# Kernel optimization log

Measured on AMD Instinct MI355X. Metric: run time of the kernel, lower is better.

Reference implementation:

```python
import jax, jax.numpy as jnp
import numpy as np

RADIUS = 4
SIGMA_I = 10.0
SIGMA_X = 4.0
NUM_CLASSES = 8
PAD = RADIUS - 1          # 3, ConstantPad3d(radius-1, eps)
WIN = 2 * PAD + 1         # 7x7x7 window
EPS = float(np.finfo(np.float64).eps)


def _dist_flat():
    # spatial gaussian, zero outside the ball x^2+y^2+z^2 < radius^2
    r = np.arange(1 - RADIUS, RADIUS)
    xx, yy, zz = np.meshgrid(r, r, r, indexing='ij')
    d2 = (xx ** 2 + yy ** 2 + zz ** 2).astype(np.float32)
    dist = np.where(d2 < RADIUS ** 2, np.exp(-d2 / SIGMA_X ** 2), 0.0).astype(np.float32)
    return jnp.asarray(dist.reshape(-1))  # flattened x-major, matches i = x*49 + y*7 + z


def setup_inputs() -> dict:
    key = jax.random.key(0)
    k1, k2 = jax.random.split(key)
    batch = jax.random.normal(k1, (4, 1, 32, 32, 32), dtype=jnp.float32)
    preds = jax.random.uniform(k2, (4, 8, 32, 32, 32), dtype=jnp.float32)
    return {"batch": batch, "preds": preds}


def reference(batch, preds):
    B, _, D, H, W = batch.shape
    K = preds.shape[1]
    pad_cfg = ((0, 0), (0, 0), (PAD, PAD), (PAD, PAD), (PAD, PAD))
    pb = jnp.pad(batch, pad_cfg, constant_values=EPS)
    pp = jnp.pad(preds, pad_cfg, constant_values=EPS)
    dist_flat = _dist_flat()
    inv_sI2 = jnp.float32(1.0 / (SIGMA_I ** 2))

    def step(carry, i):
        numer, sumw = carry
        x = i // (WIN * WIN)
        y = (i // WIN) % WIN
        z = i % WIN
        sb = jax.lax.dynamic_slice(pb, (0, 0, x, y, z), (B, 1, D, H, W))
        sp = jax.lax.dynamic_slice(pp, (0, 0, x, y, z), (B, K, D, H, W))
        # affinity = intensity gaussian * spatial gaussian for this offset
        aff = jnp.exp(-jnp.square(batch - sb) * inv_sI2) * dist_flat[i]
        return (numer + aff * sp, sumw + aff), None

    init = (jnp.zeros((B, K, D, H, W), batch.dtype),
            jnp.zeros((B, 1, D, H, W), batch.dtype))
    (numer, sumw), _ = jax.lax.scan(step, init, jnp.arange(WIN ** 3))

    assocA = jnp.sum(numer * preds, axis=(2, 3, 4))  # (B, K)
    assocV = jnp.sum(sumw * preds, axis=(2, 3, 4))   # (B, K)
    return NUM_CLASSES - jnp.sum(assocA / assocV, axis=-1)  # (B,)
```

## Files before the change

kernel.cpp:

```cpp
#include <hip/hip_runtime.h>
#include <hip/hip_fp16.h>


#define EPS_F 2.220446049250313e-16f

constexpr int TD = 4, TH = 4, TW = 8;
constexpr int HD = 7, HH = 10, HW = 14;
constexpr int HVOL = HD * HH * HW;
constexpr int SXB = 168;
constexpr int SYB = 16;
constexpr int NB  = 6 * SXB + 9 * SYB + 13 + 1;
constexpr int NT = 256;
constexpr int NBLK = 1024;

#define EX0 1.0f
#define EX1 0.93941306281347578611f
#define EX4 0.77880078307140486825f
#define EX9 0.56978282473092302544f

#define K1F (-0.014426950408889634f)
#define K2F (-0.09016844005556021f)

struct Ent { int off; float lw; };
struct Tab { Ent e[64]; int n; };

constexpr Tab make_tab(int half) {
    Tab t{};
    t.n = 0;
    for (int dxq = 0; dxq < 4; ++dxq)
        for (int dyi = 0; dyi < 7; ++dyi)
            for (int dzi = 0; dzi < 7; ++dzi) {
                int dy = dyi - 3, dz = dzi - 3;
                if (dxq == 0) {
                    if (dy < 0) continue;
                    if (dy == 0 && dz <= 0) continue;
                }
                int c2 = dxq * dxq + dy * dy + dz * dz;
                if (c2 >= 16) continue;
                if (((dyi + dzi) & 1) != half) continue;
                t.e[t.n].off = dxq * SXB + dy * SYB + dz;
                t.e[t.n].lw  = (float)c2 * K2F;
                ++t.n;
            }
    return t;
}

constexpr Tab TAB0 = make_tab(0);
constexpr Tab TAB1 = make_tab(1);

template <int HALF>
__device__ __forceinline__ void accum_pairs(const float* __restrict__ sB,
                                            const uint4* __restrict__ sPk,
                                            int vown, float b_own,
                                            float acc[9]) {
    constexpr Tab T = HALF ? TAB1 : TAB0;
    constexpr int N = HALF ? TAB1.n : TAB0.n;
    constexpr int N4 = (N / 4) * 4;

#pragma unroll
    for (int i = 0; i < N4; i += 4) {
        float sb[4];
        uint4 pk[4];
#pragma unroll
        for (int j = 0; j < 4; ++j) {
            const int nv = vown + T.e[i + j].off;
            sb[j] = sB[nv];
            pk[j] = sPk[nv];
        }
#pragma unroll
        for (int j = 0; j < 4; ++j) {
            const float d = b_own - sb[j];
            const float aff =
                __builtin_amdgcn_exp2f(__builtin_fmaf(d * d, K1F, T.e[i + j].lw));
            acc[8] += aff;
            __half2 h[4];
            __builtin_memcpy(h, &pk[j], 16);
            acc[0] = __builtin_fmaf(aff, __half2float(__low2half(h[0])),  acc[0]);
            acc[1] = __builtin_fmaf(aff, __half2float(__high2half(h[0])), acc[1]);
            acc[2] = __builtin_fmaf(aff, __half2float(__low2half(h[1])),  acc[2]);
            acc[3] = __builtin_fmaf(aff, __half2float(__high2half(h[1])), acc[3]);
            acc[4] = __builtin_fmaf(aff, __half2float(__low2half(h[2])),  acc[4]);
            acc[5] = __builtin_fmaf(aff, __half2float(__high2half(h[2])), acc[5]);
            acc[6] = __builtin_fmaf(aff, __half2float(__low2half(h[3])),  acc[6]);
            acc[7] = __builtin_fmaf(aff, __half2float(__high2half(h[3])), acc[7]);
        }
    }
#pragma unroll
    for (int i = N4; i < N; ++i) {
        const int nv = vown + T.e[i].off;
        const float sb = sB[nv];
        const uint4 pk = sPk[nv];
        const float d = b_own - sb;
        const float aff =
            __builtin_amdgcn_exp2f(__builtin_fmaf(d * d, K1F, T.e[i].lw));
        acc[8] += aff;
        __half2 h[4];
        __builtin_memcpy(h, &pk, 16);
        acc[0] = __builtin_fmaf(aff, __half2float(__low2half(h[0])),  acc[0]);
        acc[1] = __builtin_fmaf(aff, __half2float(__high2half(h[0])), acc[1]);
        acc[2] = __builtin_fmaf(aff, __half2float(__low2half(h[1])),  acc[2]);
        acc[3] = __builtin_fmaf(aff, __half2float(__high2half(h[1])), acc[3]);
        acc[4] = __builtin_fmaf(aff, __half2float(__low2half(h[2])),  acc[4]);
        acc[5] = __builtin_fmaf(aff, __half2float(__high2half(h[2])), acc[5]);
        acc[6] = __builtin_fmaf(aff, __half2float(__low2half(h[3])),  acc[6]);
        acc[7] = __builtin_fmaf(aff, __half2float(__high2half(h[3])), acc[7]);
    }
}

__global__ __launch_bounds__(NT, 4)
void softncuts_main(const float* __restrict__ batch,
                    const float* __restrict__ preds,
                    float* __restrict__ partials) {
    __shared__ float sB[NB];
    __shared__ uint4 sPk[NB];
    __shared__ float sRed[4][16];

    const int bid  = blockIdx.x;
    const int bb   = bid >> 8;
    const int tile = bid & 255;
    const int tw = tile & 3;
    const int th = (tile >> 2) & 7;
    const int td = tile >> 5;
    const int d0 = td * TD, h0 = th * TH, w0 = tw * TW;

    const int tid  = threadIdx.x;
    const int half = tid >> 7;
    const int vtid = tid & 127;
    const int lw = vtid & 7;
    const int lh = (vtid >> 3) & 3;
    const int ld = vtid >> 5;

    const float* bbase = batch + (size_t)bb * 32768;
    const float* pbase = preds + (size_t)bb * 8 * 32768;
    for (int v = tid; v < HVOL; v += NT) {
        int hw_ = v % HW;
        int t   = v / HW;
        int hh_ = t % HH;
        int hd_ = t / HH;
        int f  = hd_ * SXB + hh_ * SYB + hw_;
        int gd = d0 + hd_, gh = h0 + hh_ - 3, gw = w0 + hw_ - 3;
        bool in = ((unsigned)gd < 32u) & ((unsigned)gh < 32u) & ((unsigned)gw < 32u);
        int sidx = (gd * 32 + gh) * 32 + gw;
        sB[f] = in ? bbase[sidx] : EPS_F;
        unsigned u[4];
#pragma unroll
        for (int k = 0; k < 4; ++k) {
            float a = in ? pbase[sidx + (2 * k) * 32768]     : 0.f;
            float b = in ? pbase[sidx + (2 * k + 1) * 32768] : 0.f;
            unsigned lo = __half_as_ushort(__float2half(a));
            unsigned hi = __half_as_ushort(__float2half(b));
            u[k] = lo | (hi << 16);
        }
        sPk[f] = make_uint4(u[0], u[1], u[2], u[3]);
    }
    __syncthreads();

    const int gdo = d0 + ld, gho = h0 + lh, gwo = w0 + lw;
    const int sidx_own = (gdo * 32 + gho) * 32 + gwo;
    const float b_own = bbase[sidx_own];
    float q[8];
#pragma unroll
    for (int k = 0; k < 8; ++k) q[k] = pbase[sidx_own + k * 32768];

    const int vown = ld * SXB + (lh + 3) * SYB + (lw + 3);

    float acc[9];
#pragma unroll
    for (int i = 0; i < 9; ++i) acc[i] = 0.f;

    if (half == 0) accum_pairs<0>(sB, sPk, vown, b_own, acc);
    else           accum_pairs<1>(sB, sPk, vown, b_own, acc);

    float S = 0.f;
    const bool border = (d0 < 3) | (h0 < 3) | (h0 + TH > 29) | (w0 < 3) | (w0 + TW > 29);
    if (border && half == 0) {
        constexpr float EXT[10] = {EX0, EX1, 0.f, 0.f, EX4, 0.f, 0.f, 0.f, 0.f, EX9};
        for (int dxi = 0; dxi < 7; ++dxi) {
            const int dx  = dxi - 3;
            const int dxx = dx * dx;
            const bool ind = (unsigned)(gdo + dx) < 32u;
            for (int dyi = 0; dyi < 7; ++dyi) {
                const int dy   = dyi - 3;
                const int c2xy = dxx + dy * dy;
                if (c2xy >= 16) continue;
                const float wxy = __expf((float)c2xy * -0.0625f);
                const bool inxy = ind & ((unsigned)(gho + dy) < 32u);
#pragma unroll
                for (int dzi = 0; dzi < 7; ++dzi) {
                    const int dz  = dzi - 3;
                    const int czz = dz * dz;
                    const bool neg = (dx < 0) || (dx == 0 && (dy < 0 || (dy == 0 && dz < 0)));
                    const bool valid = ((c2xy + czz) < 16) && neg;
                    const bool inall = inxy & ((unsigned)(gwo + dz) < 32u);
                    S += (valid && !inall) ? wxy * EXT[czz] : 0.f;
                }
            }
        }
    }
    const float db = b_own - EPS_F;
    const float selfpad = (half == 0) ? (1.f + S * __expf(db * db * -0.01f)) : 0.f;

    float vals[16];
#pragma unroll
    for (int k = 0; k < 8; ++k) {
        vals[k]     = q[k] * (2.f * acc[k] + ((half == 0) ? q[k] : 0.f));
        vals[8 + k] = q[k] * (acc[8] + selfpad) + acc[k];
    }

#pragma unroll
    for (int i = 0; i < 16; ++i) {
        float s = vals[i];
        for (int off = 32; off; off >>= 1) s += __shfl_down(s, off);
        vals[i] = s;
    }
    const int wave = tid >> 6;
    const int lane = tid & 63;
    if (lane == 0) {
#pragma unroll
        for (int i = 0; i < 16; ++i) sRed[wave][i] = vals[i];
    }
    __syncthreads();
    if (tid < 16) {
        partials[tid * NBLK + bid] =
            sRed[0][tid] + sRed[1][tid] + sRed[2][tid] + sRed[3][tid];
    }
}

__global__ __launch_bounds__(1024)
void softncuts_finalize(const float* __restrict__ partials,
                        float* __restrict__ out) {
    __shared__ float red[64];
    const int tid = threadIdx.x;
    const int group = tid >> 4;
    const int j0 = tid & 15;
    const int slot = group & 15;
    const int bb = group >> 4;

    const float* p = partials + slot * NBLK + bb * 256;
    float s = 0.f;
#pragma unroll
    for (int k = 0; k < 16; ++k) s += p[j0 + 16 * k];
    for (int off = 8; off; off >>= 1) s += __shfl_down(s, off, 16);
    if (j0 == 0) red[group] = s;
    __syncthreads();

    if (tid < 4) {
        float accv = 0.f;
#pragma unroll
        for (int k = 0; k < 8; ++k)
            accv += red[tid * 16 + k] / red[tid * 16 + 8 + k];
        out[tid] = 8.0f - accv;
    }
}

extern "C" void kernel_launch(void* const* d_in, const int* in_sizes, int n_in,
                              void* d_out, int out_size, void* d_ws, size_t ws_size,
                              hipStream_t stream) {
    const float* batch = (const float*)d_in[0];
    const float* preds = (const float*)d_in[1];
    float* out      = (float*)d_out;
    float* partials = (float*)d_ws;

    softncuts_main<<<dim3(NBLK), dim3(NT), 0, stream>>>(batch, preds, partials);
    softncuts_finalize<<<dim3(1), dim3(1024), 0, stream>>>(partials, out);
}
```

Before: 85.96 us.

## Enlarge tiles to one voxel per thread and vectorize halo staging loads

Doubles the tile height so each 256-thread block covers 256 output voxels, with each thread handling all neighbour offsets instead of splitting them across two thread halves. This halves the block count and cuts the relative halo-load overhead. The halo staging loop now loads four consecutive W elements with float4 for batch and all eight pred channels when they are in bounds, falling back to scalar loads at edges. The row stride in shared memory changes to 17 to reduce bank conflicts. In exchange, each thread does twice as much serial accumulation, so there is less latency hiding and more register pressure, and the border padding correction now runs on all threads of border blocks.

```diff
diff --git a/kernel.cpp b/kernel.cpp
--- a/kernel.cpp
+++ b/kernel.cpp
@@ -4,14 +4,14 @@
 
 #define EPS_F 2.220446049250313e-16f
 
-constexpr int TD = 4, TH = 4, TW = 8;
-constexpr int HD = 7, HH = 10, HW = 14;
-constexpr int HVOL = HD * HH * HW;
-constexpr int SXB = 168;
-constexpr int SYB = 16;
-constexpr int NB  = 6 * SXB + 9 * SYB + 13 + 1;
+constexpr int TD = 4, TH = 8, TW = 8;
+constexpr int HDh = 7, HHh = 14, HWh = 14;
+constexpr int SYB = 17;
+constexpr int SXB = HHh * SYB;
+constexpr int NB  = 6 * SXB + 13 * SYB + 13 + 1;
 constexpr int NT = 256;
-constexpr int NBLK = 1024;
+constexpr int NBLK = 512;
+constexpr int NTASK = HDh * HHh * 4;
 
 #define EX0 1.0f
 #define EX1 0.93941306281347578611f
@@ -22,9 +22,9 @@
 #define K2F (-0.09016844005556021f)
 
 struct Ent { int off; float lw; };
-struct Tab { Ent e[64]; int n; };
-
-constexpr Tab make_tab(int half) {
+struct Tab { Ent e[128]; int n; };
+
+constexpr Tab make_tab() {
     Tab t{};
     t.n = 0;
     for (int dxq = 0; dxq < 4; ++dxq)
@@ -37,33 +37,115 @@
                 }
                 int c2 = dxq * dxq + dy * dy + dz * dz;
                 if (c2 >= 16) continue;
-                if (((dyi + dzi) & 1) != half) continue;
                 t.e[t.n].off = dxq * SXB + dy * SYB + dz;
                 t.e[t.n].lw  = (float)c2 * K2F;
                 ++t.n;
             }
     return t;
 }
-
-constexpr Tab TAB0 = make_tab(0);
-constexpr Tab TAB1 = make_tab(1);
-
-template <int HALF>
-__device__ __forceinline__ void accum_pairs(const float* __restrict__ sB,
-                                            const uint4* __restrict__ sPk,
-                                            int vown, float b_own,
-                                            float acc[9]) {
-    constexpr Tab T = HALF ? TAB1 : TAB0;
-    constexpr int N = HALF ? TAB1.n : TAB0.n;
-    constexpr int N4 = (N / 4) * 4;
-
+constexpr Tab TAB = make_tab();
+
+__device__ __forceinline__ unsigned pack2(float a, float b) {
+    return (unsigned)__half_as_ushort(__float2half(a)) |
+           ((unsigned)__half_as_ushort(__float2half(b)) << 16);
+}
+
+__global__ __launch_bounds__(NT, 4)
+void softncuts_main(const float* __restrict__ batch,
+                    const float* __restrict__ preds,
+                    float* __restrict__ partials) {
+    __shared__ float sB[NB];
+    __shared__ uint4 sPk[NB];
+    __shared__ float sRed[4][16];
+
+    const int bid  = blockIdx.x;
+    const int bb   = bid >> 7;
+    const int tile = bid & 127;
+    const int tw = tile & 3;
+    const int th = (tile >> 2) & 3;
+    const int td = tile >> 4;
+    const int d0 = td * TD, h0 = th * TH, w0 = tw * TW;
+
+    const int tid = threadIdx.x;
+    const int lw = tid & 7;
+    const int lh = (tid >> 3) & 7;
+    const int ld = tid >> 6;
+
+    const float* bbase = batch + (size_t)bb * 32768;
+    const float* pbase = preds + (size_t)bb * 8 * 32768;
+
+    for (int t = tid; t < NTASK; t += NT) {
+        const int c   = t & 3;
+        const int row = t >> 2;
+        const int hh  = row % HHh;
+        const int hd  = row / HHh;
+        const int gd  = d0 + hd;
+        const int gh  = h0 + hh - 3;
+        const int gw0 = w0 - 4 + c * 4;
+        const int hwb = c * 4 - 1;
+        const bool fast = (gd < 32) & ((unsigned)gh < 32u) & (gw0 >= 0) & (gw0 + 3 < 32);
+        if (fast) {
+            const int sidx = (gd * 32 + gh) * 32 + gw0;
+            float4 pv[9];
+            pv[0] = *(const float4*)(bbase + sidx);
+#pragma unroll
+            for (int k = 0; k < 8; ++k)
+                pv[k + 1] = *(const float4*)(pbase + sidx + k * 32768);
+#pragma unroll
+            for (int e = 0; e < 4; ++e) {
+                const int hw = hwb + e;
+                if (hw < 0 || hw >= HWh) continue;
+                const int f = hd * SXB + hh * SYB + hw;
+                sB[f] = ((const float*)&pv[0])[e];
+                unsigned u[4];
+#pragma unroll
+                for (int k = 0; k < 4; ++k)
+                    u[k] = pack2(((const float*)&pv[2 * k + 1])[e],
+                                 ((const float*)&pv[2 * k + 2])[e]);
+                sPk[f] = make_uint4(u[0], u[1], u[2], u[3]);
+            }
+        } else {
+#pragma unroll
+            for (int e = 0; e < 4; ++e) {
+                const int hw = hwb + e;
+                if (hw < 0 || hw >= HWh) continue;
+                const int gw = gw0 + e;
+                const bool in = (gd < 32) & ((unsigned)gh < 32u) & ((unsigned)gw < 32u);
+                const int sidx = (gd * 32 + gh) * 32 + gw;
+                const int f = hd * SXB + hh * SYB + hw;
+                sB[f] = in ? bbase[sidx] : EPS_F;
+                unsigned u[4];
+#pragma unroll
+                for (int k = 0; k < 4; ++k)
+                    u[k] = pack2(in ? pbase[sidx + (2 * k) * 32768]     : 0.f,
+                                 in ? pbase[sidx + (2 * k + 1) * 32768] : 0.f);
+                sPk[f] = make_uint4(u[0], u[1], u[2], u[3]);
+            }
+        }
+    }
+    __syncthreads();
+
+    const int gdo = d0 + ld, gho = h0 + lh, gwo = w0 + lw;
+    const int sidx_own = (gdo * 32 + gho) * 32 + gwo;
+    const float b_own = bbase[sidx_own];
+    float q[8];
+#pragma unroll
+    for (int k = 0; k < 8; ++k) q[k] = pbase[sidx_own + k * 32768];
+
+    const int vown = ld * SXB + (lh + 3) * SYB + (lw + 3);
+
+    float acc[9];
+#pragma unroll
+    for (int i = 0; i < 9; ++i) acc[i] = 0.f;
+
+    constexpr int N = TAB.n, N4 = (N / 4) * 4;
 #pragma unroll
     for (int i = 0; i < N4; i += 4) {
         float sb[4];
         uint4 pk[4];
 #pragma unroll
         for (int j = 0; j < 4; ++j) {
-            const int nv = vown + T.e[i + j].off;
+            const int nv = vown + TAB.e[i + j].off;
             sb[j] = sB[nv];
             pk[j] = sPk[nv];
         }
@@ -71,7 +153,7 @@
         for (int j = 0; j < 4; ++j) {
             const float d = b_own - sb[j];
             const float aff =
-                __builtin_amdgcn_exp2f(__builtin_fmaf(d * d, K1F, T.e[i + j].lw));
+                __builtin_amdgcn_exp2f(__builtin_fmaf(d * d, K1F, TAB.e[i + j].lw));
             acc[8] += aff;
             __half2 h[4];
             __builtin_memcpy(h, &pk[j], 16);
@@ -87,12 +169,12 @@
     }
 #pragma unroll
     for (int i = N4; i < N; ++i) {
-        const int nv = vown + T.e[i].off;
+        const int nv = vown + TAB.e[i].off;
         const float sb = sB[nv];
         const uint4 pk = sPk[nv];
         const float d = b_own - sb;
         const float aff =
-            __builtin_amdgcn_exp2f(__builtin_fmaf(d * d, K1F, T.e[i].lw));
+            __builtin_amdgcn_exp2f(__builtin_fmaf(d * d, K1F, TAB.e[i].lw));
         acc[8] += aff;
         __half2 h[4];
         __builtin_memcpy(h, &pk, 16);
@@ -105,75 +187,10 @@
         acc[6] = __builtin_fmaf(aff, __half2float(__low2half(h[3])),  acc[6]);
         acc[7] = __builtin_fmaf(aff, __half2float(__high2half(h[3])), acc[7]);
     }
-}
-
-__global__ __launch_bounds__(NT, 4)
-void softncuts_main(const float* __restrict__ batch,
-                    const float* __restrict__ preds,
-                    float* __restrict__ partials) {
-    __shared__ float sB[NB];
-    __shared__ uint4 sPk[NB];
-    __shared__ float sRed[4][16];
-
-    const int bid  = blockIdx.x;
-    const int bb   = bid >> 8;
-    const int tile = bid & 255;
-    const int tw = tile & 3;
-    const int th = (tile >> 2) & 7;
-    const int td = tile >> 5;
-    const int d0 = td * TD, h0 = th * TH, w0 = tw * TW;
-
-    const int tid  = threadIdx.x;
-    const int half = tid >> 7;
-    const int vtid = tid & 127;
-    const int lw = vtid & 7;
-    const int lh = (vtid >> 3) & 3;
-    const int ld = vtid >> 5;
-
-    const float* bbase = batch + (size_t)bb * 32768;
-    const float* pbase = preds + (size_t)bb * 8 * 32768;
-    for (int v = tid; v < HVOL; v += NT) {
-        int hw_ = v % HW;
-        int t   = v / HW;
-        int hh_ = t % HH;
-        int hd_ = t / HH;
-        int f  = hd_ * SXB + hh_ * SYB + hw_;
-        int gd = d0 + hd_, gh = h0 + hh_ - 3, gw = w0 + hw_ - 3;
-        bool in = ((unsigned)gd < 32u) & ((unsigned)gh < 32u) & ((unsigned)gw < 32u);
-        int sidx = (gd * 32 + gh) * 32 + gw;
-        sB[f] = in ? bbase[sidx] : EPS_F;
-        unsigned u[4];
-#pragma unroll
-        for (int k = 0; k < 4; ++k) {
-            float a = in ? pbase[sidx + (2 * k) * 32768]     : 0.f;
-            float b = in ? pbase[sidx + (2 * k + 1) * 32768] : 0.f;
-            unsigned lo = __half_as_ushort(__float2half(a));
-            unsigned hi = __half_as_ushort(__float2half(b));
-            u[k] = lo | (hi << 16);
-        }
-        sPk[f] = make_uint4(u[0], u[1], u[2], u[3]);
-    }
-    __syncthreads();
-
-    const int gdo = d0 + ld, gho = h0 + lh, gwo = w0 + lw;
-    const int sidx_own = (gdo * 32 + gho) * 32 + gwo;
-    const float b_own = bbase[sidx_own];
-    float q[8];
-#pragma unroll
-    for (int k = 0; k < 8; ++k) q[k] = pbase[sidx_own + k * 32768];
-
-    const int vown = ld * SXB + (lh + 3) * SYB + (lw + 3);
-
-    float acc[9];
-#pragma unroll
-    for (int i = 0; i < 9; ++i) acc[i] = 0.f;
-
-    if (half == 0) accum_pairs<0>(sB, sPk, vown, b_own, acc);
-    else           accum_pairs<1>(sB, sPk, vown, b_own, acc);
 
     float S = 0.f;
     const bool border = (d0 < 3) | (h0 < 3) | (h0 + TH > 29) | (w0 < 3) | (w0 + TW > 29);
-    if (border && half == 0) {
+    if (border) {
         constexpr float EXT[10] = {EX0, EX1, 0.f, 0.f, EX4, 0.f, 0.f, 0.f, 0.f, EX9};
         for (int dxi = 0; dxi < 7; ++dxi) {
             const int dx  = dxi - 3;
@@ -198,12 +215,12 @@
         }
     }
     const float db = b_own - EPS_F;
-    const float selfpad = (half == 0) ? (1.f + S * __expf(db * db * -0.01f)) : 0.f;
+    const float selfpad = 1.f + S * __expf(db * db * -0.01f);
 
     float vals[16];
 #pragma unroll
     for (int k = 0; k < 8; ++k) {
-        vals[k]     = q[k] * (2.f * acc[k] + ((half == 0) ? q[k] : 0.f));
+        vals[k]     = q[k] * (2.f * acc[k] + q[k]);
         vals[8 + k] = q[k] * (acc[8] + selfpad) + acc[k];
     }
 
@@ -236,10 +253,10 @@
     const int slot = group & 15;
     const int bb = group >> 4;
 
-    const float* p = partials + slot * NBLK + bb * 256;
+    const float* p = partials + slot * NBLK + bb * 128;
     float s = 0.f;
 #pragma unroll
-    for (int k = 0; k < 16; ++k) s += p[j0 + 16 * k];
+    for (int k = 0; k < 8; ++k) s += p[j0 + 16 * k];
     for (int off = 8; off; off >>= 1) s += __shfl_down(s, off, 16);
     if (j0 == 0) red[group] = s;
     __syncthreads();
```

Measured after the change: 191.1 us. 2.22x slower.
